# Kernel tuning notes

Measured on AMD Instinct MI355X. Metric: run time of the kernel, lower is better.

The kernel has to match this reference:

```python
import jax, jax.numpy as jnp
import numpy as np

EPS = 1e-5

def _conv3x3(x, w):
    # x: [B,C,H,W], w: [O,I,3,3], stride 1, padding 1
    return jax.lax.conv_general_dilated(
        x, w, window_strides=(1, 1), padding=((1, 1), (1, 1)),
        dimension_numbers=('NCHW', 'OIHW', 'NCHW'))

def _bn(x, gamma, beta, mean, var):
    inv = gamma / jnp.sqrt(var + EPS)
    return x * inv[None, :, None, None] + (beta - mean * inv)[None, :, None, None]

def setup_inputs() -> dict:
    key = jax.random.key(0)
    ks = jax.random.split(key, 6)
    B, C, H, W, E = 32, 64, 112, 112, 10
    x = jax.random.normal(ks[0], (B, C, H, W), dtype=jnp.float32)
    w1 = jax.random.normal(ks[1], (E, C, C, 3, 3), dtype=jnp.float32) * 0.05
    w2 = jax.random.normal(ks[2], (E, C, C, 3, 3), dtype=jnp.float32) * 0.05
    alpha = jax.random.uniform(ks[3], (E,), dtype=jnp.float32)
    return {
        'x': x, 'w1': w1, 'w2': w2, 'alpha': alpha,
        'bn1_gamma': jnp.ones((C,), jnp.float32),
        'bn1_beta': jnp.zeros((C,), jnp.float32),
        'bn1_mean': jnp.zeros((C,), jnp.float32),
        'bn1_var': jax.random.uniform(ks[4], (C,), jnp.float32) + 0.5,
        'bn2_gamma': jnp.ones((C,), jnp.float32),
        'bn2_beta': jnp.zeros((C,), jnp.float32),
        'bn2_mean': jnp.zeros((C,), jnp.float32),
        'bn2_var': jax.random.uniform(ks[5], (C,), jnp.float32) + 0.5,
    }

def reference(x, w1, w2, alpha,
              bn1_gamma, bn1_beta, bn1_mean, bn1_var,
              bn2_gamma, bn2_beta, bn2_mean, bn2_var):
    # Convolution is linear in its weights, so sum_i alpha[i] * conv(x, w_i)
    # == conv(x, sum_i alpha[i] * w_i): pre-combine experts into one kernel.
    w1_eff = jnp.einsum('e,eoihw->oihw', alpha, w1)
    w2_eff = jnp.einsum('e,eoihw->oihw', alpha, w2)
    out = _conv3x3(x, w1_eff)
    out = jax.nn.relu(_bn(out, bn1_gamma, bn1_beta, bn1_mean, bn1_var))
    out = _conv3x3(out, w2_eff)
    out = _bn(out, bn2_gamma, bn2_beta, bn2_mean, bn2_var)
    return jax.nn.relu(out + x)
```

## Files before the change

kernel.cpp:

```cpp
#include <hip/hip_runtime.h>


typedef __bf16 bf16x8 __attribute__((ext_vector_type(8)));
typedef float f32x4 __attribute__((ext_vector_type(4)));
typedef unsigned short u16;
typedef u16 u16x8 __attribute__((ext_vector_type(8)));

#define NH 112
#define NW 112
#define PH 114
#define PW 114
#define PROWB (PW * 128)
#define BUFB 23040

#define WAITVM(n) asm volatile("s_waitcnt vmcnt(" #n ")" ::: "memory")
#define SCHEDB __builtin_amdgcn_sched_barrier(0)

__device__ __forceinline__ u16 f2b(float f) {
  unsigned u = __builtin_bit_cast(unsigned, f);
  u += 0x7FFFu + ((u >> 16) & 1u);
  return (u16)(u >> 16);
}
__device__ __forceinline__ float b2f(u16 b) {
  unsigned u = ((unsigned)b) << 16;
  return __builtin_bit_cast(float, u);
}

__device__ __forceinline__ void gl_lds16(const void* g, void* l) {
  __builtin_amdgcn_global_load_lds(
      (const __attribute__((address_space(1))) unsigned int*)g,
      (__attribute__((address_space(3))) unsigned int*)l, 16, 0, 0);
}

__global__ void border_zero(u16* __restrict__ a, u16* __restrict__ bbuf) {
  int idx = blockIdx.x * 256 + threadIdx.x;
  if (idx >= 231424) return;
  int c8 = idx & 7;
  int t = idx >> 3;
  int buf = t >= 14464;
  t -= buf * 14464;
  int img = t / 452, e = t % 452;
  int h, w;
  if (e < 114) { h = 0; w = e; }
  else if (e < 228) { h = 113; w = e - 114; }
  else if (e < 340) { h = e - 227; w = 0; }
  else { h = e - 339; w = 113; }
  u16* base = buf ? bbuf : a;
  u16x8 z = {0, 0, 0, 0, 0, 0, 0, 0};
  *reinterpret_cast<u16x8*>(base + (((long)img * PH + h) * PW + w) * 64 + c8 * 8) = z;
}

__global__ __launch_bounds__(256) void transform_kernel(const float* __restrict__ x,
                                                        u16* __restrict__ xpad) {
  __shared__ alignas(16) u16 t[7168];
  int tid = threadIdx.x, bid = blockIdx.x;
  int b = bid / NH, h = bid % NH;
  const float* src = x + (long)b * 64 * 12544 + h * NW;
  f32x4 v[7];
#pragma unroll
  for (int it = 0; it < 7; ++it) {
    int fid = it * 256 + tid;
    int c = fid / 28, wq = fid % 28;
    v[it] = *reinterpret_cast<const f32x4*>(src + c * 12544 + wq * 4);
  }
#pragma unroll
  for (int it = 0; it < 7; ++it) {
    int fid = it * 256 + tid;
    int c = fid / 28, wq = fid % 28;
    int key = (wq & 7) << 4;
#pragma unroll
    for (int j = 0; j < 4; ++j) {
      int px = wq * 4 + j;
      *reinterpret_cast<u16*>((char*)t + px * 128 + ((c * 2) ^ key)) = f2b(v[it][j]);
    }
  }
  __syncthreads();
  int hp = h + 1;
  u16* rowb = xpad + (((long)b * PH + hp) * PW) * 64;
#pragma unroll
  for (int it = 0; it < 4; ++it) {
    int cidx = it * 256 + tid;
    if (cidx < 896) {
      int c8 = cidx & 7, px = cidx >> 3;
      int lchunk = c8 ^ ((px >> 2) & 7);
      u16x8 vv = *reinterpret_cast<const u16x8*>((const char*)t + px * 128 + lchunk * 16);
      int wp = px + 1;
      int gkey = (2 * hp + wp) & 7;
      *reinterpret_cast<u16x8*>(rowb + (long)wp * 64 + ((c8 ^ gkey) * 8)) = vv;
    }
  }
}

__global__ void prep_kernel(
    const float* __restrict__ w1, const float* __restrict__ w2,
    const float* __restrict__ alpha,
    const float* __restrict__ g1, const float* __restrict__ b1,
    const float* __restrict__ m1, const float* __restrict__ v1,
    const float* __restrict__ g2, const float* __restrict__ b2,
    const float* __restrict__ m2, const float* __restrict__ v2,
    u16* __restrict__ weff1, u16* __restrict__ weff2, float* __restrict__ bnc) {
  int idx = blockIdx.x * 256 + threadIdx.x;
  if (idx < 36864) {
    int i = idx & 63;
    int o = (idx >> 6) & 63;
    int kpos = idx >> 12;
    int base = (o * 64 + i) * 9 + kpos;
    float a1 = 0.f, a2 = 0.f;
#pragma unroll
    for (int e = 0; e < 10; ++e) {
      float al = alpha[e];
      a1 += al * w1[e * 36864 + base];
      a2 += al * w2[e * 36864 + base];
    }
    weff1[idx] = f2b(a1);
    weff2[idx] = f2b(a2);
  }
  if (blockIdx.x == 0 && threadIdx.x < 64) {
    int c = threadIdx.x;
    float i1 = g1[c] * rsqrtf(v1[c] + 1e-5f);
    float i2 = g2[c] * rsqrtf(v2[c] + 1e-5f);
    bnc[c] = i1;
    bnc[64 + c] = b1[c] - m1[c] * i1;
    bnc[128 + c] = i2;
    bnc[192 + c] = b2[c] - m2[c] * i2;
  }
}

__global__ __launch_bounds__(256, 2) void conv_p0_kernel(
    const u16* __restrict__ xin, const u16* __restrict__ weff,
    const float* __restrict__ bnc, u16* __restrict__ ypad) {
  __shared__ alignas(64) char smem[2 * BUFB];

  int tid = threadIdx.x, lane = tid & 63, wv = tid >> 6;
  int ol = lane & 15, kg = (lane >> 4) & 3;
  const int o = wv * 16 + ol;

  float inv = bnc[o];
  float bias = bnc[64 + o];

  bf16x8 wf[3][3][2];
#pragma unroll
  for (int kh = 0; kh < 3; ++kh)
#pragma unroll
    for (int kw = 0; kw < 3; ++kw)
#pragma unroll
      for (int ks = 0; ks < 2; ++ks)
        wf[kh][kw][ks] = __builtin_bit_cast(
            bf16x8, *reinterpret_cast<const u16x8*>(
                        weff + (((kh * 3 + kw) * 64 + o) * 64 + ks * 32 + kg * 8)));
  asm volatile("s_waitcnt vmcnt(0)" ::: "memory");
  SCHEDB;

  int sb = (blockIdx.x & 7) * 196 + (blockIdx.x >> 3);
  int tb[2], th0[2], tw0[2];
#pragma unroll
  for (int t = 0; t < 2; ++t) {
    int tt = sb * 2 + t;
    tb[t] = tt / 98;
    int r = tt % 98;
    th0[t] = (r / 7) * 8;
    tw0[t] = (r % 7) * 16;
  }

  auto stage = [&](int t, int boff) {
#pragma unroll
    for (int k = 0; k < 6; ++k) {
      int i = wv + k * 4;
      if (i < 23) {
        int cb = i * 64 + lane;
        if (cb < 1440) {
          int row = cb / 144, rem = cb % 144;
          gl_lds16((const char*)(xin + (((long)tb[t] * PH + th0[t]) * PW + tw0[t]) * 64) +
                       (long)row * PROWB + rem * 16,
                   smem + boff + cb * 16);
        }
      }
    }
  };

  stage(0, 0);
  asm volatile("" ::: "memory");
  stage(1, BUFB);
  asm volatile("" ::: "memory");
  if (wv < 3) WAITVM(6);
  else        WAITVM(5);
  SCHEDB;

#pragma unroll
  for (int t = 0; t < 2; ++t) {
    const int boff = t * BUFB;
    __builtin_amdgcn_s_barrier();
    SCHEDB;

    f32x4 acc[8];
#pragma unroll
    for (int mf = 0; mf < 8; ++mf) acc[mf] = f32x4{0.f, 0.f, 0.f, 0.f};

#pragma unroll
    for (int kw = 0; kw < 3; ++kw)
#pragma unroll
      for (int ks = 0; ks < 2; ++ks) {
        const int col = ol + kw;
        const int sb8 = (ks << 2) | kg;
        bf16x8 a[4];
#pragma unroll
        for (int u = 0; u < 3; ++u) {
          int slot = sb8 ^ ((2 * u + col) & 7);
          a[u] = *reinterpret_cast<const bf16x8*>(smem + boff + (u * 18 + col) * 128 +
                                                  slot * 16);
        }
#pragma unroll
        for (int mf = 0; mf < 8; ++mf) {
          if (mf < 7) {
            int rr = mf + 3;
            int slot = sb8 ^ ((2 * rr + col) & 7);
            a[(mf + 3) & 3] = *reinterpret_cast<const bf16x8*>(
                smem + boff + (rr * 18 + col) * 128 + slot * 16);
          }
          acc[mf] = __builtin_amdgcn_mfma_f32_16x16x32_bf16(a[mf & 3], wf[0][kw][ks],
                                                            acc[mf], 0, 0, 0);
          acc[mf] = __builtin_amdgcn_mfma_f32_16x16x32_bf16(a[(mf + 1) & 3], wf[1][kw][ks],
                                                            acc[mf], 0, 0, 0);
          acc[mf] = __builtin_amdgcn_mfma_f32_16x16x32_bf16(a[(mf + 2) & 3], wf[2][kw][ks],
                                                            acc[mf], 0, 0, 0);
        }
      }

    if (t == 0) {
      asm volatile("s_waitcnt vmcnt(0)" ::: "memory");
      SCHEDB;
    }

    SCHEDB;
    __builtin_amdgcn_s_barrier();
    SCHEDB;
    u16* ys = reinterpret_cast<u16*>(smem + boff);
#pragma unroll
    for (int mf = 0; mf < 8; ++mf)
#pragma unroll
      for (int rg = 0; rg < 4; ++rg) {
        int p = mf * 16 + kg * 4 + rg;
        ys[p * 72 + o] = f2b(fmaxf(acc[mf][rg] * inv + bias, 0.f));
      }
    asm volatile("s_waitcnt lgkmcnt(0)" ::: "memory");
    SCHEDB;
    __builtin_amdgcn_s_barrier();
    SCHEDB;
#pragma unroll
    for (int it = 0; it < 4; ++it) {
      int cidx = it * 256 + tid;
      int c8 = cidx & 7, p = cidx >> 3;
      int hp = th0[t] + (p >> 4) + 1, wp = tw0[t] + (p & 15) + 1;
      int gkey = (2 * hp + wp) & 7;
      *reinterpret_cast<u16x8*>(ypad + (((long)tb[t] * PH + hp) * PW + wp) * 64 +
                                ((c8 ^ gkey) * 8)) =
          *reinterpret_cast<const u16x8*>(ys + p * 72 + c8 * 8);
    }
  }
}

template <int RESID>
__global__ __launch_bounds__(256, 2) void conv_p1_kernel(
    const u16* __restrict__ yin, const float* __restrict__ x,
    const u16* __restrict__ xres, const u16* __restrict__ weff,
    const float* __restrict__ bnc, float* __restrict__ out) {
  constexpr int BUF = RESID ? (BUFB + 16384) : BUFB;
  __shared__ alignas(64) char smem[2 * BUF];

  int tid = threadIdx.x, lane = tid & 63, wv = tid >> 6;
  int ol = lane & 15, kg = (lane >> 4) & 3;
  const int o = wv * 16 + ol;

  float inv = bnc[128 + o];
  float bias = bnc[192 + o];

  bf16x8 wf[3][3][2];
#pragma unroll
  for (int kh = 0; kh < 3; ++kh)
#pragma unroll
    for (int kw = 0; kw < 3; ++kw)
#pragma unroll
      for (int ks = 0; ks < 2; ++ks)
        wf[kh][kw][ks] = __builtin_bit_cast(
            bf16x8, *reinterpret_cast<const u16x8*>(
                        weff + (((kh * 3 + kw) * 64 + o) * 64 + ks * 32 + kg * 8)));
  asm volatile("s_waitcnt vmcnt(0)" ::: "memory");
  SCHEDB;

  int sb = (blockIdx.x & 7) * 98 + (blockIdx.x >> 3);
  int tb[4], th0[4], tw0[4];
#pragma unroll
  for (int t = 0; t < 4; ++t) {
    int tt = sb * 4 + t;
    tb[t] = tt / 98;
    int r = tt % 98;
    th0[t] = (r / 7) * 8;
    tw0[t] = (r % 7) * 16;
  }

  auto stage = [&](int t, int boff) {
#pragma unroll
    for (int k = 0; k < 6; ++k) {
      int i = wv + k * 4;
      if (i < 23) {
        int cb = i * 64 + lane;
        if (cb < 1440) {
          int row = cb / 144, rem = cb % 144;
          gl_lds16((const char*)(yin + (((long)tb[t] * PH + th0[t]) * PW + tw0[t]) * 64) +
                       (long)row * PROWB + rem * 16,
                   smem + boff + cb * 16);
        }
      }
    }
    if constexpr (RESID) {
#pragma unroll
      for (int k = 0; k < 4; ++k) {
        int i = wv + k * 4;
        int cr = i * 64 + lane;
        int rp = cr >> 7, rem = cr & 127;
        gl_lds16((const char*)xres +
                     (((long)tb[t] * PH + th0[t] + 1 + rp) * PW + tw0[t] + 1) * 128 +
                     rem * 16,
                 smem + boff + BUFB + cr * 16);
      }
    }
  };
  auto gateS = [&] {
    if constexpr (RESID) {
      if (wv < 3) WAITVM(10); else WAITVM(9);
    } else {
      if (wv < 3) WAITVM(6); else WAITVM(5);
    }
  };

  stage(0, 0);
  asm volatile("" ::: "memory");
  stage(1, BUF);
  asm volatile("" ::: "memory");
  gateS();
  SCHEDB;

#pragma unroll
  for (int t = 0; t < 4; ++t) {
    const int boff = (t & 1) * BUF;
    __builtin_amdgcn_s_barrier();
    SCHEDB;

    f32x4 acc[8];
#pragma unroll
    for (int mf = 0; mf < 8; ++mf) acc[mf] = f32x4{0.f, 0.f, 0.f, 0.f};

#pragma unroll
    for (int kw = 0; kw < 3; ++kw)
#pragma unroll
      for (int ks = 0; ks < 2; ++ks) {
        const int col = ol + kw;
        const int sb8 = (ks << 2) | kg;
        bf16x8 a[4];
#pragma unroll
        for (int u = 0; u < 3; ++u) {
          int slot = sb8 ^ ((2 * u + col) & 7);
          a[u] = *reinterpret_cast<const bf16x8*>(smem + boff + (u * 18 + col) * 128 +
                                                  slot * 16);
        }
#pragma unroll
        for (int mf = 0; mf < 8; ++mf) {
          if (mf < 7) {
            int rr = mf + 3;
            int slot = sb8 ^ ((2 * rr + col) & 7);
            a[(mf + 3) & 3] = *reinterpret_cast<const bf16x8*>(
                smem + boff + (rr * 18 + col) * 128 + slot * 16);
          }
          acc[mf] = __builtin_amdgcn_mfma_f32_16x16x32_bf16(a[mf & 3], wf[0][kw][ks],
                                                            acc[mf], 0, 0, 0);
          acc[mf] = __builtin_amdgcn_mfma_f32_16x16x32_bf16(a[(mf + 1) & 3], wf[1][kw][ks],
                                                            acc[mf], 0, 0, 0);
          acc[mf] = __builtin_amdgcn_mfma_f32_16x16x32_bf16(a[(mf + 2) & 3], wf[2][kw][ks],
                                                            acc[mf], 0, 0, 0);
        }
      }

    if constexpr (RESID) {
#pragma unroll
      for (int mf = 0; mf < 8; ++mf) {
        int h = th0[t] + mf, hp = h + 1;
        f32x4 vv;
#pragma unroll
        for (int rg = 0; rg < 4; ++rg) {
          int wq = kg * 4 + rg, wp = tw0[t] + wq + 1;
          int key = (2 * hp + wp) & 7;
          u16 bv = *reinterpret_cast<const u16*>(
              smem + boff + BUFB + (mf * 16 + wq) * 128 + (((o >> 3) ^ key) * 16) +
              (o & 7) * 2);
          vv[rg] = fmaxf(acc[mf][rg] * inv + bias + b2f(bv), 0.f);
        }
        *reinterpret_cast<f32x4*>(out + (((tb[t] * 64 + o) * NH + h) * NW + tw0[t] +
                                         kg * 4)) = vv;
      }
    } else {
#pragma unroll
      for (int half = 0; half < 2; ++half) {
        f32x4 xr[4];
#pragma unroll
        for (int m = 0; m < 4; ++m) {
          int h = th0[t] + half * 4 + m;
          xr[m] = *reinterpret_cast<const f32x4*>(
              x + (((tb[t] * 64 + o) * NH + h) * NW + tw0[t] + kg * 4));
        }
#pragma unroll
        for (int m = 0; m < 4; ++m) {
          int mf = half * 4 + m;
          int h = th0[t] + mf;
          f32x4 vv;
#pragma unroll
          for (int rg = 0; rg < 4; ++rg)
            vv[rg] = fmaxf(acc[mf][rg] * inv + bias + xr[m][rg], 0.f);
          *reinterpret_cast<f32x4*>(
              out + (((tb[t] * 64 + o) * NH + h) * NW + tw0[t] + kg * 4)) = vv;
        }
      }
    }

    SCHEDB;
    __builtin_amdgcn_s_barrier();
    SCHEDB;
    if (t + 2 < 4) stage(t + 2, boff);
    if (t < 2) {
      gateS();
    } else if (t == 2) {
      WAITVM(0);
    }
    SCHEDB;
  }
}

extern "C" void kernel_launch(void* const* d_in, const int* in_sizes, int n_in,
                              void* d_out, int out_size, void* d_ws, size_t ws_size,
                              hipStream_t stream) {
  const float* x = (const float*)d_in[0];
  const float* w1 = (const float*)d_in[1];
  const float* w2 = (const float*)d_in[2];
  const float* alpha = (const float*)d_in[3];
  const float* g1 = (const float*)d_in[4];
  const float* b1 = (const float*)d_in[5];
  const float* m1 = (const float*)d_in[6];
  const float* v1 = (const float*)d_in[7];
  const float* g2 = (const float*)d_in[8];
  const float* b2 = (const float*)d_in[9];
  const float* m2 = (const float*)d_in[10];
  const float* v2 = (const float*)d_in[11];
  float* out = (float*)d_out;

  char* ws = (char*)d_ws;
  u16* weff1 = (u16*)ws;
  u16* weff2 = (u16*)(ws + 73728);
  float* bnc = (float*)(ws + 147456);
  u16* y1pad = (u16*)(ws + 148480);
  const size_t PADB = 53231616ull;
  bool big = ws_size >= 148480ull + 2ull * PADB;
  u16* xpad = big ? (u16*)(ws + 148480 + PADB) : (u16*)d_out;

  border_zero<<<904, 256, 0, stream>>>(xpad, y1pad);
  transform_kernel<<<32 * NH, 256, 0, stream>>>(x, xpad);
  prep_kernel<<<144, 256, 0, stream>>>(w1, w2, alpha, g1, b1, m1, v1,
                                       g2, b2, m2, v2, weff1, weff2, bnc);
  conv_p0_kernel<<<1568, 256, 0, stream>>>(xpad, weff1, bnc, y1pad);
  if (big)
    conv_p1_kernel<1><<<784, 256, 0, stream>>>(y1pad, x, xpad, weff2, bnc, out);
  else
    conv_p1_kernel<0><<<784, 256, 0, stream>>>(y1pad, x, nullptr, weff2, bnc, out);
}
```

Baseline: 133.9 us.

## Make both conv kernels persistent with strided tile loop over 512 blocks

Replaces the fixed per-block tile counts (2 tiles in conv_p0, 4 in conv_p1) with a persistent grid of 512 blocks. Each block walks tiles with stride 512 and double-buffers the LDS staging across iterations. The goal is to load the weight fragments into registers once per block and to keep the prefetch pipeline running over more tiles, cutting launch and prologue overhead. In exchange, tile counts per block become uneven (6 or 7), which can leave a tail imbalance, and the loop is no longer fully unrolled.

```diff
diff --git a/kernel.cpp b/kernel.cpp
--- a/kernel.cpp
+++ b/kernel.cpp
@@ -12,6 +12,7 @@
 #define PW 114
 #define PROWB (PW * 128)
 #define BUFB 23040
+#define NTILES 3136
 
 #define WAITVM(n) asm volatile("s_waitcnt vmcnt(" #n ")" ::: "memory")
 #define SCHEDB __builtin_amdgcn_sched_barrier(0)
@@ -151,18 +152,14 @@
   asm volatile("s_waitcnt vmcnt(0)" ::: "memory");
   SCHEDB;
 
-  int sb = (blockIdx.x & 7) * 196 + (blockIdx.x >> 3);
-  int tb[2], th0[2], tw0[2];
-#pragma unroll
-  for (int t = 0; t < 2; ++t) {
-    int tt = sb * 2 + t;
-    tb[t] = tt / 98;
+  const int sb = (blockIdx.x & 7) * 64 + (blockIdx.x >> 3);
+  const int n = (NTILES - sb + 511) >> 9;
+
+  auto stage = [&](int tt, int boff) {
+    int b = tt / 98;
     int r = tt % 98;
-    th0[t] = (r / 7) * 8;
-    tw0[t] = (r % 7) * 16;
-  }
-
-  auto stage = [&](int t, int boff) {
+    int h0 = (r / 7) * 8, w0 = (r % 7) * 16;
+    const char* src = (const char*)(xin + (((long)b * PH + h0) * PW + w0) * 64);
 #pragma unroll
     for (int k = 0; k < 6; ++k) {
       int i = wv + k * 4;
@@ -170,25 +167,27 @@
         int cb = i * 64 + lane;
         if (cb < 1440) {
           int row = cb / 144, rem = cb % 144;
-          gl_lds16((const char*)(xin + (((long)tb[t] * PH + th0[t]) * PW + tw0[t]) * 64) +
-                       (long)row * PROWB + rem * 16,
-                   smem + boff + cb * 16);
+          gl_lds16(src + (long)row * PROWB + rem * 16, smem + boff + cb * 16);
         }
       }
     }
   };
 
-  stage(0, 0);
+  stage(sb, 0);
   asm volatile("" ::: "memory");
-  stage(1, BUFB);
+  stage(sb + 512, BUFB);
   asm volatile("" ::: "memory");
   if (wv < 3) WAITVM(6);
   else        WAITVM(5);
   SCHEDB;
 
-#pragma unroll
-  for (int t = 0; t < 2; ++t) {
-    const int boff = t * BUFB;
+  for (int j = 0; j < n; ++j) {
+    const int boff = (j & 1) * BUFB;
+    const int tt = sb + (j << 9);
+    const int b = tt / 98;
+    const int r = tt % 98;
+    const int th0 = (r / 7) * 8, tw0 = (r % 7) * 16;
+
     __builtin_amdgcn_s_barrier();
     SCHEDB;
 
@@ -226,11 +225,6 @@
         }
       }
 
-    if (t == 0) {
-      asm volatile("s_waitcnt vmcnt(0)" ::: "memory");
-      SCHEDB;
-    }
-
     SCHEDB;
     __builtin_amdgcn_s_barrier();
     SCHEDB;
@@ -250,11 +244,25 @@
     for (int it = 0; it < 4; ++it) {
       int cidx = it * 256 + tid;
       int c8 = cidx & 7, p = cidx >> 3;
-      int hp = th0[t] + (p >> 4) + 1, wp = tw0[t] + (p & 15) + 1;
+      int hp = th0 + (p >> 4) + 1, wp = tw0 + (p & 15) + 1;
       int gkey = (2 * hp + wp) & 7;
-      *reinterpret_cast<u16x8*>(ypad + (((long)tb[t] * PH + hp) * PW + wp) * 64 +
+      *reinterpret_cast<u16x8*>(ypad + (((long)b * PH + hp) * PW + wp) * 64 +
                                 ((c8 ^ gkey) * 8)) =
           *reinterpret_cast<const u16x8*>(ys + p * 72 + c8 * 8);
+    }
+
+    if (j + 1 < n) {
+      SCHEDB;
+      __builtin_amdgcn_s_barrier();
+      SCHEDB;
+      if (j + 2 < n) {
+        stage(sb + ((j + 2) << 9), boff);
+        if (wv < 3) WAITVM(6);
+        else        WAITVM(5);
+      } else {
+        WAITVM(0);
+      }
+      SCHEDB;
     }
   }
 }
@@ -287,18 +295,14 @@
   asm volatile("s_waitcnt vmcnt(0)" ::: "memory");
   SCHEDB;
 
-  int sb = (blockIdx.x & 7) * 98 + (blockIdx.x >> 3);
-  int tb[4], th0[4], tw0[4];
-#pragma unroll
-  for (int t = 0; t < 4; ++t) {
-    int tt = sb * 4 + t;
-    tb[t] = tt / 98;
+  const int sb = (blockIdx.x & 7) * 64 + (blockIdx.x >> 3);
+  const int n = (NTILES - sb + 511) >> 9;
+
+  auto stage = [&](int tt, int boff) {
+    int b = tt / 98;
     int r = tt % 98;
-    th0[t] = (r / 7) * 8;
-    tw0[t] = (r % 7) * 16;
-  }
-
-  auto stage = [&](int t, int boff) {
+    int h0 = (r / 7) * 8, w0 = (r % 7) * 16;
+    const char* src = (const char*)(yin + (((long)b * PH + h0) * PW + w0) * 64);
 #pragma unroll
     for (int k = 0; k < 6; ++k) {
       int i = wv + k * 4;
@@ -306,9 +310,7 @@
         int cb = i * 64 + lane;
         if (cb < 1440) {
           int row = cb / 144, rem = cb % 144;
-          gl_lds16((const char*)(yin + (((long)tb[t] * PH + th0[t]) * PW + tw0[t]) * 64) +
-                       (long)row * PROWB + rem * 16,
-                   smem + boff + cb * 16);
+          gl_lds16(src + (long)row * PROWB + rem * 16, smem + boff + cb * 16);
         }
       }
     }
@@ -318,8 +320,7 @@
         int i = wv + k * 4;
         int cr = i * 64 + lane;
         int rp = cr >> 7, rem = cr & 127;
-        gl_lds16((const char*)xres +
-                     (((long)tb[t] * PH + th0[t] + 1 + rp) * PW + tw0[t] + 1) * 128 +
+        gl_lds16((const char*)xres + (((long)b * PH + h0 + 1 + rp) * PW + w0 + 1) * 128 +
                      rem * 16,
                  smem + boff + BUFB + cr * 16);
       }
@@ -333,16 +334,20 @@
     }
   };
 
-  stage(0, 0);
+  stage(sb, 0);
   asm volatile("" ::: "memory");
-  stage(1, BUF);
+  stage(sb + 512, BUF);
   asm volatile("" ::: "memory");
   gateS();
   SCHEDB;
 
-#pragma unroll
-  for (int t = 0; t < 4; ++t) {
-    const int boff = (t & 1) * BUF;
+  for (int j = 0; j < n; ++j) {
+    const int boff = (j & 1) * BUF;
+    const int tt = sb + (j << 9);
+    const int b = tt / 98;
+    const int r = tt % 98;
+    const int th0 = (r / 7) * 8, tw0 = (r % 7) * 16;
+
     __builtin_amdgcn_s_barrier();
     SCHEDB;
 
@@ -383,19 +388,19 @@
     if constexpr (RESID) {
 #pragma unroll
       for (int mf = 0; mf < 8; ++mf) {
-        int h = th0[t] + mf, hp = h + 1;
+        int h = th0 + mf, hp = h + 1;
         f32x4 vv;
 #pragma unroll
         for (int rg = 0; rg < 4; ++rg) {
-          int wq = kg * 4 + rg, wp = tw0[t] + wq + 1;
+          int wq = kg * 4 + rg, wp = tw0 + wq + 1;
           int key = (2 * hp + wp) & 7;
           u16 bv = *reinterpret_cast<const u16*>(
               smem + boff + BUFB + (mf * 16 + wq) * 128 + (((o >> 3) ^ key) * 16) +
               (o & 7) * 2);
           vv[rg] = fmaxf(acc[mf][rg] * inv + bias + b2f(bv), 0.f);
         }
-        *reinterpret_cast<f32x4*>(out + (((tb[t] * 64 + o) * NH + h) * NW + tw0[t] +
-                                         kg * 4)) = vv;
+        *reinterpret_cast<f32x4*>(out + (((b * 64 + o) * NH + h) * NW + tw0 + kg * 4)) =
+            vv;
       }
     } else {
 #pragma unroll
@@ -403,34 +408,36 @@
         f32x4 xr[4];
 #pragma unroll
         for (int m = 0; m < 4; ++m) {
-          int h = th0[t] + half * 4 + m;
+          int h = th0 + half * 4 + m;
           xr[m] = *reinterpret_cast<const f32x4*>(
-              x + (((tb[t] * 64 + o) * NH + h) * NW + tw0[t] + kg * 4));
+              x + (((b * 64 + o) * NH + h) * NW + tw0 + kg * 4));
         }
 #pragma unroll
         for (int m = 0; m < 4; ++m) {
           int mf = half * 4 + m;
-          int h = th0[t] + mf;
+          int h = th0 + mf;
           f32x4 vv;
 #pragma unroll
           for (int rg = 0; rg < 4; ++rg)
             vv[rg] = fmaxf(acc[mf][rg] * inv + bias + xr[m][rg], 0.f);
-          *reinterpret_cast<f32x4*>(
-              out + (((tb[t] * 64 + o) * NH + h) * NW + tw0[t] + kg * 4)) = vv;
-        }
-      }
-    }
-
-    SCHEDB;
-    __builtin_amdgcn_s_barrier();
-    SCHEDB;
-    if (t + 2 < 4) stage(t + 2, boff);
-    if (t < 2) {
-      gateS();
-    } else if (t == 2) {
-      WAITVM(0);
-    }
-    SCHEDB;
+          *reinterpret_cast<f32x4*>(out + (((b * 64 + o) * NH + h) * NW + tw0 + kg * 4)) =
+              vv;
+        }
+      }
+    }
+
+    if (j + 1 < n) {
+      SCHEDB;
+      __builtin_amdgcn_s_barrier();
+      SCHEDB;
+      if (j + 2 < n) {
+        stage(sb + ((j + 2) << 9), boff);
+        gateS();
+      } else {
+        WAITVM(0);
+      }
+      SCHEDB;
+    }
   }
 }
 
@@ -464,9 +471,9 @@
   transform_kernel<<<32 * NH, 256, 0, stream>>>(x, xpad);
   prep_kernel<<<144, 256, 0, stream>>>(w1, w2, alpha, g1, b1, m1, v1,
                                        g2, b2, m2, v2, weff1, weff2, bnc);
-  conv_p0_kernel<<<1568, 256, 0, stream>>>(xpad, weff1, bnc, y1pad);
+  conv_p0_kernel<<<512, 256, 0, stream>>>(xpad, weff1, bnc, y1pad);
   if (big)
-    conv_p1_kernel<1><<<784, 256, 0, stream>>>(y1pad, x, xpad, weff2, bnc, out);
+    conv_p1_kernel<1><<<512, 256, 0, stream>>>(y1pad, x, xpad, weff2, bnc, out);
   else
-    conv_p1_kernel<0><<<784, 256, 0, stream>>>(y1pad, x, nullptr, weff2, bnc, out);
-}
+    conv_p1_kernel<0><<<512, 256, 0, stream>>>(y1pad, x, nullptr, weff2, bnc, out);
+}
```

Measured after the change: 119.5 us (median of 2 runs). 10.7% less time.
